# Optimization experiments

Hardware: AMD Instinct MI355X
Metric: run time of the kernel (lower is better)

## Reference

```python
import jax, jax.numpy as jnp
import numpy as np

N = 50000          # nodes
E = 1250000        # edges (avg degree 25)
EMBED = 64
HIDS = [64, 64, 64]
EDGE_DIM = 7       # 1 + 6
VOCAB = 5 ** 8     # 390625
NEG_SLOPE = 0.01   # F.leaky_relu default


def setup_inputs() -> dict:
    key = jax.random.key(0)
    ks = jax.random.split(key, 14)
    L = len(HIDS)
    x = jax.random.randint(ks[0], (N,), 0, VOCAB)
    edge_index = jax.random.randint(ks[1], (2, E), 0, N)
    edge_attr = jax.random.normal(ks[2], (E, EDGE_DIM), dtype=jnp.float32)
    emb = jax.random.normal(ks[3], (VOCAB, EMBED), dtype=jnp.float32) * 0.02
    # all layers have in = out = 64, so params are stacked along layer axis
    lin1_w = jax.random.normal(ks[4], (L, EMBED + EDGE_DIM, HIDS[0]), dtype=jnp.float32) * 0.1
    att_l = jax.random.normal(ks[5], (L, HIDS[0]), dtype=jnp.float32) * 0.1
    att_r = jax.random.normal(ks[6], (L, EMBED), dtype=jnp.float32) * 0.1
    lin2_w = jax.random.normal(ks[7], (L, HIDS[0], HIDS[0]), dtype=jnp.float32) * 0.1
    gbias = jax.random.normal(ks[8], (L, HIDS[0]), dtype=jnp.float32) * 0.01
    d_cat = int(np.sum(HIDS)) + EMBED  # 256
    fc1_w = jax.random.normal(ks[9], (d_cat, 20), dtype=jnp.float32) * 0.05
    fc1_b = jax.random.normal(ks[10], (20,), dtype=jnp.float32) * 0.01
    fc2_w = jax.random.normal(ks[11], (20, 1), dtype=jnp.float32) * 0.1
    fc2_b = jax.random.normal(ks[12], (1,), dtype=jnp.float32) * 0.01
    return {"x": x, "edge_index": edge_index, "edge_attr": edge_attr, "emb": emb,
            "lin1_w": lin1_w, "att_l": att_l, "att_r": att_r, "lin2_w": lin2_w,
            "gbias": gbias, "fc1_w": fc1_w, "fc1_b": fc1_b, "fc2_w": fc2_w, "fc2_b": fc2_b}


def _gate_conv(h, src, dst, edge_attr, w1, al, ar, w2, b):
    # message from source j -> target i; attention softmax over edges sharing a target
    xj = jnp.concatenate([h[src], edge_attr], axis=-1)            # [E, in+7]
    xj = jax.nn.leaky_relu(xj @ w1, NEG_SLOPE)                    # [E, out]
    alpha = jax.nn.leaky_relu(jnp.sum(xj * al, -1) + jnp.sum(h[dst] * ar, -1), NEG_SLOPE)
    amax = jax.ops.segment_max(alpha, dst, num_segments=N)        # [N]
    ea = jnp.exp(alpha - amax[dst])                               # [E]
    denom = jax.ops.segment_sum(ea, dst, num_segments=N)          # [N]
    a = ea / (denom[dst] + 1e-16)
    msg = (xj @ w2) * a[:, None]                                  # [E, out]
    return jax.ops.segment_sum(msg, dst, num_segments=N) + b      # [N, out]


def reference(x, edge_index, edge_attr, emb, lin1_w, att_l, att_r, lin2_w,
              gbias, fc1_w, fc1_b, fc2_w, fc2_b):
    src, dst = edge_index[0], edge_index[1]
    h = emb[x]                                                    # [N, EMBED]
    feats = [h]
    for l in range(len(HIDS)):
        h = jax.nn.relu(_gate_conv(h, src, dst, edge_attr,
                                   lin1_w[l], att_l[l], att_r[l], lin2_w[l], gbias[l]))
        feats.append(h)
    hcat = jnp.concatenate(feats, axis=-1)                        # [N, 256]
    z = jax.nn.relu(hcat @ fc1_w + fc1_b)
    out = jax.nn.sigmoid(z @ fc2_w + fc2_b)
    return out.squeeze(-1)                                        # [N]
```

## Files before the change

kernel.cpp:

```cpp
#include <hip/hip_runtime.h>
#include <math.h>

#define NEG 0.01f

typedef _Float16 f16;
typedef f16 h2 __attribute__((ext_vector_type(2)));

__device__ __forceinline__ float lrelu(float x) { return x > 0.f ? x : NEG * x; }

__device__ __forceinline__ h2 lrelu2(h2 x) {
    h2 y = x * (f16)0.01f;
    return __builtin_elementwise_max(x, y);
}

__device__ __forceinline__ float q16_allsum(float v) {
    int x;
    x = __builtin_amdgcn_update_dpp(0, __float_as_int(v), 0xB1, 0xF, 0xF, true);  v += __int_as_float(x);
    x = __builtin_amdgcn_update_dpp(0, __float_as_int(v), 0x4E, 0xF, 0xF, true);  v += __int_as_float(x);
    x = __builtin_amdgcn_update_dpp(0, __float_as_int(v), 0x124, 0xF, 0xF, true); v += __int_as_float(x);
    x = __builtin_amdgcn_update_dpp(0, __float_as_int(v), 0x128, 0xF, 0xF, true); v += __int_as_float(x);
    return v;
}

__device__ __forceinline__ float x16_32_sum(float v) {
    v += __int_as_float(__builtin_amdgcn_ds_swizzle(__float_as_int(v), 0x401F));
    v += __shfl_xor(v, 32, 64);
    return v;
}

__global__ void k_zero(int* deg, int n) {
    int i = blockIdx.x * blockDim.x + threadIdx.x;
    if (i < n) deg[i] = 0;
}

__global__ void k_count(const int* __restrict__ dst, int* __restrict__ deg,
                        int* __restrict__ rank, int E) {
    int e = blockIdx.x * blockDim.x + threadIdx.x;
    if (e < E) rank[e] = atomicAdd(&deg[dst[e]], 1);
}

__global__ __launch_bounds__(256) void k_scan_part(const int* __restrict__ deg,
                                                   int* __restrict__ bsum, int n) {
    __shared__ int sh[256];
    int b = blockIdx.x, t = threadIdx.x;
    int i0 = b * 1024 + t * 4;
    int s = 0;
    if (i0 + 3 < n) { int4 v = *(const int4*)(deg + i0); s = v.x + v.y + v.z + v.w; }
    else { for (int k = 0; k < 4; k++) if (i0 + k < n) s += deg[i0 + k]; }
    sh[t] = s; __syncthreads();
    for (int d = 128; d > 0; d >>= 1) { if (t < d) sh[t] += sh[t + d]; __syncthreads(); }
    if (t == 0) bsum[b] = sh[0];
}

__global__ __launch_bounds__(256) void k_scan_out(const int* __restrict__ deg,
                                                  const int* __restrict__ bsum,
                                                  int* __restrict__ off, int nb, int n) {
    __shared__ int sb[256];
    __shared__ int sh[256];
    int b = blockIdx.x, t = threadIdx.x;
    int v = (t < nb) ? bsum[t] : 0;
    sb[t] = v; __syncthreads();
    for (int d = 1; d < 256; d <<= 1) {
        int u = (t >= d) ? sb[t - d] : 0;
        __syncthreads(); sb[t] += u; __syncthreads();
    }
    int base = (b == 0) ? 0 : sb[b - 1];
    if (b == 0 && t == 0) off[n] = sb[255];
    int i0 = b * 1024 + t * 4;
    int4 v4 = make_int4(0, 0, 0, 0);
    if (i0 + 3 < n) v4 = *(const int4*)(deg + i0);
    else {
        v4.x = (i0     < n) ? deg[i0]     : 0;
        v4.y = (i0 + 1 < n) ? deg[i0 + 1] : 0;
        v4.z = (i0 + 2 < n) ? deg[i0 + 2] : 0;
        v4.w = (i0 + 3 < n) ? deg[i0 + 3] : 0;
    }
    int s = v4.x + v4.y + v4.z + v4.w;
    sh[t] = s; __syncthreads();
    for (int d = 1; d < 256; d <<= 1) {
        int u = (t >= d) ? sh[t - d] : 0;
        __syncthreads(); sh[t] += u; __syncthreads();
    }
    int ex = base + sh[t] - s;
    if (i0     < n) off[i0]     = ex;
    if (i0 + 1 < n) off[i0 + 1] = ex + v4.x;
    if (i0 + 2 < n) off[i0 + 2] = ex + v4.x + v4.y;
    if (i0 + 3 < n) off[i0 + 3] = ex + v4.x + v4.y + v4.z;
}

__global__ void k_fill_embed(const int* __restrict__ src, const int* __restrict__ dst,
                             const float* __restrict__ eattr, const int* __restrict__ off,
                             const int* __restrict__ rank, uint4* __restrict__ rec, int E,
                             int nbE,
                             const int* __restrict__ x, const float* __restrict__ emb,
                             float* __restrict__ hcat, int N) {
    if ((int)blockIdx.x < nbE) {
        int e = blockIdx.x * 256 + threadIdx.x;
        if (e >= E) return;
        int slot = off[dst[e]] + rank[e];
        const float* ap = eattr + (size_t)e * 7;
        float a0 = ap[0], a1 = ap[1], a2 = ap[2], a3 = ap[3], a4 = ap[4], a5 = ap[5], a6 = ap[6];
        uint4 rv;
        h2 p01 = { (f16)a0, (f16)a1 };
        h2 p23 = { (f16)a2, (f16)a3 };
        h2 p45 = { (f16)a4, (f16)a5 };
        rv.x = __builtin_bit_cast(unsigned int, p01);
        rv.y = __builtin_bit_cast(unsigned int, p23);
        rv.z = __builtin_bit_cast(unsigned int, p45);
        unsigned int a6b = (unsigned int)__builtin_bit_cast(unsigned short, (f16)a6);
        rv.w = a6b | ((unsigned int)src[e] << 16);
        rec[slot] = rv;
    } else {
        int idx = ((int)blockIdx.x - nbE) * 256 + threadIdx.x;
        int node = idx >> 4, j4 = (idx & 15) * 4;
        if (node < N) {
            float4 v = *(const float4*)(emb + (size_t)x[node] * 64 + j4);
            *(float4*)(hcat + (size_t)node * 256 + j4) = v;
        }
    }
}

__global__ __launch_bounds__(256) void k_gemm64(
    const float* __restrict__ A, int a_stride,
    const float* __restrict__ B, const float* __restrict__ bias,
    float* __restrict__ C, int c_stride, f16* __restrict__ Ch,
    int N, int do_relu,
    const float* __restrict__ ar, float* __restrict__ r_out)
{
    __shared__ __align__(16) float sA[64][132];
    __shared__ __align__(16) float sB[64 * 64];
    __shared__ float sar[64];
    int tid = threadIdx.x;
    int row0 = blockIdx.x * 128;

    {
        const float4* b4 = (const float4*)B;
        float4* s4 = (float4*)sB;
        for (int i = tid; i < 1024; i += 256) s4[i] = b4[i];
    }
    if (ar && tid < 64) sar[tid] = ar[tid];

#pragma unroll
    for (int pass = 0; pass < 8; ++pass) {
        int nl = pass * 16 + (tid & 15);
        int k4 = (tid >> 4) * 4;
        int n = row0 + nl; if (n >= N) n = N - 1;
        float4 v = *(const float4*)(A + (size_t)n * a_stride + k4);
        sA[k4 + 0][nl] = v.x; sA[k4 + 1][nl] = v.y;
        sA[k4 + 2][nl] = v.z; sA[k4 + 3][nl] = v.w;
    }
    __syncthreads();

    int tr = tid >> 4, tc = tid & 15;
    int r0 = tr * 8, c0 = tc * 4;
    float acc[8][4];
#pragma unroll
    for (int i = 0; i < 8; i++)
#pragma unroll
        for (int j = 0; j < 4; j++) acc[i][j] = 0.f;

#pragma unroll 4
    for (int k = 0; k < 64; ++k) {
        float4 b4 = *(const float4*)(sB + k * 64 + c0);
        float4 a0 = *(const float4*)&sA[k][r0];
        float4 a1 = *(const float4*)&sA[k][r0 + 4];
#pragma unroll
        for (int j = 0; j < 4; j++) {
            float bj = (&b4.x)[j];
            acc[0][j] += a0.x * bj; acc[1][j] += a0.y * bj;
            acc[2][j] += a0.z * bj; acc[3][j] += a0.w * bj;
            acc[4][j] += a1.x * bj; acc[5][j] += a1.y * bj;
            acc[6][j] += a1.z * bj; acc[7][j] += a1.w * bj;
        }
    }

    float4 bv = make_float4(0.f, 0.f, 0.f, 0.f);
    if (bias) bv = *(const float4*)(bias + c0);
#pragma unroll
    for (int i = 0; i < 8; i++) {
        int n = row0 + r0 + i;
        if (n < N) {
            float4 o;
            o.x = acc[i][0] + bv.x; o.y = acc[i][1] + bv.y;
            o.z = acc[i][2] + bv.z; o.w = acc[i][3] + bv.w;
            if (do_relu) {
                o.x = fmaxf(o.x, 0.f); o.y = fmaxf(o.y, 0.f);
                o.z = fmaxf(o.z, 0.f); o.w = fmaxf(o.w, 0.f);
            }
            if (C) *(float4*)(C + (size_t)n * c_stride + c0) = o;
            if (Ch) {
                uint2 gw;
                gw.x = __builtin_bit_cast(unsigned int, __builtin_amdgcn_cvt_pkrtz(o.x, o.y));
                gw.y = __builtin_bit_cast(unsigned int, __builtin_amdgcn_cvt_pkrtz(o.z, o.w));
                *(uint2*)(Ch + (size_t)n * 64 + c0) = gw;
            }
        }
    }

    if (r_out && tid < 128) {
        int n = row0 + tid;
        if (n < N) {
            float racc = 0.f;
#pragma unroll
            for (int k = 0; k < 64; k++) racc += sA[k][tid] * sar[k];
            r_out[n] = racc;
        }
    }
}

__global__ __launch_bounds__(256) void k_gemm2g1(
    float* __restrict__ hc,
    const float* __restrict__ W2, const float* __restrict__ bias,
    const float* __restrict__ W1n, const float* __restrict__ arn,
    f16* __restrict__ g, float* __restrict__ r_out, int N)
{
    __shared__ __align__(16) float sA[64][132];
    __shared__ __align__(16) float sB[64 * 64];
    __shared__ float sar[64];
    int tid = threadIdx.x, row0 = blockIdx.x * 128;

    {
        const float4* b4 = (const float4*)W2;
        float4* s4 = (float4*)sB;
        for (int i = tid; i < 1024; i += 256) s4[i] = b4[i];
    }
    if (tid < 64) sar[tid] = arn[tid];

#pragma unroll
    for (int pass = 0; pass < 8; ++pass) {
        int nl = pass * 16 + (tid & 15);
        int k4 = (tid >> 4) * 4;
        int n = row0 + nl; if (n >= N) n = N - 1;
        float4 v = *(const float4*)(hc + (size_t)n * 256 + k4);
        sA[k4 + 0][nl] = v.x; sA[k4 + 1][nl] = v.y;
        sA[k4 + 2][nl] = v.z; sA[k4 + 3][nl] = v.w;
    }
    __syncthreads();

    int tr = tid >> 4, tc = tid & 15;
    int r0 = tr * 8, c0 = tc * 4;
    float acc[8][4];
#pragma unroll
    for (int i = 0; i < 8; i++)
#pragma unroll
        for (int j = 0; j < 4; j++) acc[i][j] = 0.f;

#pragma unroll 4
    for (int k = 0; k < 64; ++k) {
        float4 b4 = *(const float4*)(sB + k * 64 + c0);
        float4 a0 = *(const float4*)&sA[k][r0];
        float4 a1 = *(const float4*)&sA[k][r0 + 4];
#pragma unroll
        for (int j = 0; j < 4; j++) {
            float bj = (&b4.x)[j];
            acc[0][j] += a0.x * bj; acc[1][j] += a0.y * bj;
            acc[2][j] += a0.z * bj; acc[3][j] += a0.w * bj;
            acc[4][j] += a1.x * bj; acc[5][j] += a1.y * bj;
            acc[6][j] += a1.z * bj; acc[7][j] += a1.w * bj;
        }
    }

    float4 bv = *(const float4*)(bias + c0);
#pragma unroll
    for (int i = 0; i < 8; i++) {
        acc[i][0] = fmaxf(acc[i][0] + bv.x, 0.f);
        acc[i][1] = fmaxf(acc[i][1] + bv.y, 0.f);
        acc[i][2] = fmaxf(acc[i][2] + bv.z, 0.f);
        acc[i][3] = fmaxf(acc[i][3] + bv.w, 0.f);
        int n = row0 + r0 + i;
        if (n < N) *(float4*)(hc + (size_t)n * 256 + c0) =
            make_float4(acc[i][0], acc[i][1], acc[i][2], acc[i][3]);
    }
    __syncthreads();

    {
        const float4* b4 = (const float4*)W1n;
        float4* s4 = (float4*)sB;
        for (int i = tid; i < 1024; i += 256) s4[i] = b4[i];
    }
#pragma unroll
    for (int i = 0; i < 8; i++)
#pragma unroll
        for (int j = 0; j < 4; j++) sA[c0 + j][r0 + i] = acc[i][j];
    __syncthreads();

#pragma unroll
    for (int i = 0; i < 8; i++)
#pragma unroll
        for (int j = 0; j < 4; j++) acc[i][j] = 0.f;

#pragma unroll 4
    for (int k = 0; k < 64; ++k) {
        float4 b4 = *(const float4*)(sB + k * 64 + c0);
        float4 a0 = *(const float4*)&sA[k][r0];
        float4 a1 = *(const float4*)&sA[k][r0 + 4];
#pragma unroll
        for (int j = 0; j < 4; j++) {
            float bj = (&b4.x)[j];
            acc[0][j] += a0.x * bj; acc[1][j] += a0.y * bj;
            acc[2][j] += a0.z * bj; acc[3][j] += a0.w * bj;
            acc[4][j] += a1.x * bj; acc[5][j] += a1.y * bj;
            acc[6][j] += a1.z * bj; acc[7][j] += a1.w * bj;
        }
    }

#pragma unroll
    for (int i = 0; i < 8; i++) {
        int n = row0 + r0 + i;
        if (n < N) {
            uint2 gw;
            gw.x = __builtin_bit_cast(unsigned int, __builtin_amdgcn_cvt_pkrtz(acc[i][0], acc[i][1]));
            gw.y = __builtin_bit_cast(unsigned int, __builtin_amdgcn_cvt_pkrtz(acc[i][2], acc[i][3]));
            *(uint2*)(g + (size_t)n * 64 + c0) = gw;
        }
    }
    if (tid < 128) {
        int n = row0 + tid;
        if (n < N) {
            float racc = 0.f;
#pragma unroll
            for (int k = 0; k < 64; k++) racc += sA[k][tid] * sar[k];
            r_out[n] = racc;
        }
    }
}

struct ConvW {
    h2 w01[4], w23[4], w45[4], w6_[4];
    h2 al01, al23;
};

__device__ __forceinline__ void do_edge(uint4 rv, bool valid, float ri,
                                        const ConvW& W, const f16* __restrict__ g,
                                        int l16, float4& s, float& den) {
    h2 a01 = __builtin_bit_cast(h2, rv.x);
    h2 a23 = __builtin_bit_cast(h2, rv.y);
    h2 a45 = __builtin_bit_cast(h2, rv.z);
    h2 a6p = __builtin_bit_cast(h2, rv.w & 0xFFFFu);
    int sn  = (int)(rv.w >> 16);
    uint2 gv = *(const uint2*)(g + (size_t)sn * 64 + 4 * l16);
    h2 g01 = __builtin_bit_cast(h2, gv.x);
    h2 g23 = __builtin_bit_cast(h2, gv.y);

    float c0 = __builtin_amdgcn_fdot2(a01, W.w01[0],
               __builtin_amdgcn_fdot2(a23, W.w23[0],
               __builtin_amdgcn_fdot2(a45, W.w45[0],
               __builtin_amdgcn_fdot2(a6p, W.w6_[0], 0.f, false), false), false), false);
    float c1 = __builtin_amdgcn_fdot2(a01, W.w01[1],
               __builtin_amdgcn_fdot2(a23, W.w23[1],
               __builtin_amdgcn_fdot2(a45, W.w45[1],
               __builtin_amdgcn_fdot2(a6p, W.w6_[1], 0.f, false), false), false), false);
    float c2 = __builtin_amdgcn_fdot2(a01, W.w01[2],
               __builtin_amdgcn_fdot2(a23, W.w23[2],
               __builtin_amdgcn_fdot2(a45, W.w45[2],
               __builtin_amdgcn_fdot2(a6p, W.w6_[2], 0.f, false), false), false), false);
    float c3 = __builtin_amdgcn_fdot2(a01, W.w01[3],
               __builtin_amdgcn_fdot2(a23, W.w23[3],
               __builtin_amdgcn_fdot2(a45, W.w45[3],
               __builtin_amdgcn_fdot2(a6p, W.w6_[3], 0.f, false), false), false), false);

    h2 x01 = lrelu2(g01 + __builtin_amdgcn_cvt_pkrtz(c0, c1));
    h2 x23 = lrelu2(g23 + __builtin_amdgcn_cvt_pkrtz(c2, c3));
    float p = __builtin_amdgcn_fdot2(x01, W.al01,
              __builtin_amdgcn_fdot2(x23, W.al23, 0.f, false), false);
    p = q16_allsum(p);
    float alpha = lrelu(p + ri);
    float w = valid ? __expf(alpha) : 0.f;
    s.x += w * (float)x01.x; s.y += w * (float)x01.y;
    s.z += w * (float)x23.x; s.w += w * (float)x23.y;
    den += w;
}

__global__ __launch_bounds__(256) void k_conv(
    const int* __restrict__ off, const uint4* __restrict__ rec,
    const f16* __restrict__ g, const float* __restrict__ r,
    const float* __restrict__ w1, const float* __restrict__ al,
    float* __restrict__ aggdst, int N)
{
    int lane = threadIdx.x & 63;
    int wid  = threadIdx.x >> 6;
    int node = blockIdx.x * 4 + wid;
    if (node >= N) return;
    int q = lane >> 4, l16 = lane & 15;

    ConvW W;
    const float* wb = w1 + 64 * 64;
#pragma unroll
    for (int j = 0; j < 4; j++) {
        int f = 4 * l16 + j;
        W.w01[j] = h2{ (f16)wb[f],       (f16)wb[64 + f]  };
        W.w23[j] = h2{ (f16)wb[128 + f], (f16)wb[192 + f] };
        W.w45[j] = h2{ (f16)wb[256 + f], (f16)wb[320 + f] };
        W.w6_[j] = h2{ (f16)wb[384 + f], (f16)0.f         };
    }
    W.al01 = h2{ (f16)al[4 * l16],     (f16)al[4 * l16 + 1] };
    W.al23 = h2{ (f16)al[4 * l16 + 2], (f16)al[4 * l16 + 3] };

    float ri = r[node];
    int e0 = off[node], e1 = off[node + 1];

    float4 s = make_float4(0.f, 0.f, 0.f, 0.f);
    float den = 0.f;
    for (int e = e0; e < e1; e += 8) {
        int ea = e + q, eb = e + 4 + q;
        bool va = ea < e1, vb = eb < e1;
        uint4 ra = rec[va ? ea : (e1 - 1)];
        uint4 rb = rec[vb ? eb : (e1 - 1)];
        do_edge(ra, va, ri, W, g, l16, s, den);
        do_edge(rb, vb, ri, W, g, l16, s, den);
    }
    s.x = x16_32_sum(s.x); s.y = x16_32_sum(s.y);
    s.z = x16_32_sum(s.z); s.w = x16_32_sum(s.w);
    den = x16_32_sum(den);
    float inv = 1.f / (den + 1e-16f);
    if (q == 0) {
        float4 o = make_float4(s.x * inv, s.y * inv, s.z * inv, s.w * inv);
        *(float4*)(aggdst + (size_t)node * 256 + 4 * l16) = o;
    }
}

__global__ void k_head(const float* __restrict__ hcat, const float* __restrict__ f1w,
                       const float* __restrict__ f1b, const float* __restrict__ f2w,
                       const float* __restrict__ f2b, float* __restrict__ out, int N) {
    int i = blockIdx.x * blockDim.x + threadIdx.x;
    if (i >= N) return;
    float z[20];
#pragma unroll
    for (int j = 0; j < 20; j++) z[j] = f1b[j];
    const float4* hr = (const float4*)(hcat + (size_t)i * 256);
    for (int k4 = 0; k4 < 64; k4++) {
        float4 h = hr[k4];
        const float* wr = f1w + k4 * 4 * 20;
#pragma unroll
        for (int j = 0; j < 20; j++)
            z[j] += h.x * wr[j] + h.y * wr[20 + j] + h.z * wr[40 + j] + h.w * wr[60 + j];
    }
    float o = f2b[0];
#pragma unroll
    for (int j = 0; j < 20; j++) o += fmaxf(z[j], 0.f) * f2w[j];
    out[i] = 1.f / (1.f + __expf(-o));
}

extern "C" void kernel_launch(void* const* d_in, const int* in_sizes, int n_in,
                              void* d_out, int out_size, void* d_ws, size_t ws_size,
                              hipStream_t stream) {
    const int*   x     = (const int*)d_in[0];
    const int*   eidx  = (const int*)d_in[1];
    const float* eattr = (const float*)d_in[2];
    const float* emb   = (const float*)d_in[3];
    const float* lin1  = (const float*)d_in[4];
    const float* attl  = (const float*)d_in[5];
    const float* attr_ = (const float*)d_in[6];
    const float* lin2  = (const float*)d_in[7];
    const float* gbias = (const float*)d_in[8];
    const float* f1w   = (const float*)d_in[9];
    const float* f1b   = (const float*)d_in[10];
    const float* f2w   = (const float*)d_in[11];
    const float* f2b   = (const float*)d_in[12];
    float* out = (float*)d_out;

    int N = in_sizes[0];
    int E = in_sizes[1] / 2;
    const int* src = eidx;
    const int* dst = eidx + E;

    char* p = (char*)d_ws;
    auto alloc = [&](size_t bytes) { void* q = (void*)p; p += (bytes + 255) & ~(size_t)255; return q; };
    float* hcat = (float*)alloc((size_t)N * 256 * 4);
    f16*   g    = (f16*)alloc((size_t)N * 64 * 2);
    float* r    = (float*)alloc((size_t)N * 4);
    int*   off  = (int*)alloc((size_t)(N + 1) * 4);
    int*   deg  = (int*)alloc((size_t)N * 4);
    int*   rank = (int*)alloc((size_t)E * 4);
    int*   bsum = (int*)alloc(256 * 4);
    uint4* rec  = (uint4*)alloc((size_t)E * 16);

    int nbs = (N + 1023) / 1024;
    int nbE = (E + 255) / 256;
    int nbEmb = (N * 16 + 255) / 256;

    k_zero<<<(N + 255) / 256, 256, 0, stream>>>(deg, N);
    k_count<<<nbE, 256, 0, stream>>>(dst, deg, rank, E);
    k_scan_part<<<nbs, 256, 0, stream>>>(deg, bsum, N);
    k_scan_out<<<nbs, 256, 0, stream>>>(deg, bsum, off, nbs, N);
    k_fill_embed<<<nbE + nbEmb, 256, 0, stream>>>(src, dst, eattr, off, rank, rec, E,
                                                  nbE, x, emb, hcat, N);

    int nbg = (N + 127) / 128;
    int nbc = (N + 3) / 4;
    k_gemm64<<<nbg, 256, 0, stream>>>(hcat, 256, lin1, nullptr,
                                      nullptr, 0, g, N, 0, attr_, r);
    k_conv<<<nbc, 256, 0, stream>>>(off, rec, g, r, lin1, attl, hcat + 64, N);
    for (int l = 0; l < 2; l++) {
        k_gemm2g1<<<nbg, 256, 0, stream>>>(hcat + 64 * (l + 1),
                                           lin2 + (size_t)l * 4096, gbias + l * 64,
                                           lin1 + (size_t)(l + 1) * 71 * 64,
                                           attr_ + (l + 1) * 64, g, r, N);
        k_conv<<<nbc, 256, 0, stream>>>(off, rec, g, r,
                                        lin1 + (size_t)(l + 1) * 71 * 64,
                                        attl + (l + 1) * 64, hcat + 64 * (l + 2), N);
    }
    k_gemm64<<<nbg, 256, 0, stream>>>(hcat + 192, 256, lin2 + 2 * 4096, gbias + 128,
                                      hcat + 192, 256, nullptr, N, 1, nullptr, nullptr);
    k_head<<<(N + 255) / 256, 256, 0, stream>>>(hcat, f1w, f1b, f2w, f2b, out, N);
}
```

Measured before the change: 532.4 us.

## Fuse final GEMM with MLP head, prepack conv weights, deepen edge-loop prefetch

The last layer's lin2 GEMM is fused with the fc1/fc2 head into one kernel that keeps the layer-3 output in shared memory, so that slice of hcat is never written back and re-read. The head's dot products are split across two half-blocks. Per-layer conv edge weights and attention vectors are converted to packed fp16 once, inside the zero kernel, so each conv wave does 5 vector loads instead of many scalar float loads and conversions. The conv edge loop now handles 16 edges per iteration and issues all record and gather loads before the math, giving more memory-level parallelism at the cost of more registers.

```diff
diff --git a/kernel.cpp b/kernel.cpp
--- a/kernel.cpp
+++ b/kernel.cpp
@@ -28,9 +28,34 @@
     return v;
 }
 
-__global__ void k_zero(int* deg, int n) {
+__global__ void k_zero(int* __restrict__ deg, int n,
+                       const float* __restrict__ lin1, const float* __restrict__ attl,
+                       uint4* __restrict__ wpack) {
     int i = blockIdx.x * blockDim.x + threadIdx.x;
     if (i < n) deg[i] = 0;
+    if (i < 48) {
+        int l = i >> 4, t = i & 15;
+        const float* wb  = lin1 + (size_t)l * 71 * 64 + 64 * 64;
+        const float* alp = attl + l * 64;
+        unsigned int u[20];
+#pragma unroll
+        for (int j = 0; j < 4; j++) {
+            int f = 4 * t + j;
+            h2 a = { (f16)wb[f],       (f16)wb[64 + f]  }; u[j]      = __builtin_bit_cast(unsigned int, a);
+            h2 b = { (f16)wb[128 + f], (f16)wb[192 + f] }; u[4 + j]  = __builtin_bit_cast(unsigned int, b);
+            h2 c = { (f16)wb[256 + f], (f16)wb[320 + f] }; u[8 + j]  = __builtin_bit_cast(unsigned int, c);
+            h2 d = { (f16)wb[384 + f], (f16)0.f         }; u[12 + j] = __builtin_bit_cast(unsigned int, d);
+        }
+        h2 e0 = { (f16)alp[4 * t],     (f16)alp[4 * t + 1] }; u[16] = __builtin_bit_cast(unsigned int, e0);
+        h2 e1 = { (f16)alp[4 * t + 2], (f16)alp[4 * t + 3] }; u[17] = __builtin_bit_cast(unsigned int, e1);
+        u[18] = 0; u[19] = 0;
+        uint4* o = wpack + (size_t)i * 5;
+        o[0] = make_uint4(u[0],  u[1],  u[2],  u[3]);
+        o[1] = make_uint4(u[4],  u[5],  u[6],  u[7]);
+        o[2] = make_uint4(u[8],  u[9],  u[10], u[11]);
+        o[3] = make_uint4(u[12], u[13], u[14], u[15]);
+        o[4] = make_uint4(u[16], u[17], u[18], u[19]);
+    }
 }
 
 __global__ void k_count(const int* __restrict__ dst, int* __restrict__ deg,
@@ -330,15 +355,12 @@
     h2 al01, al23;
 };
 
-__device__ __forceinline__ void do_edge(uint4 rv, bool valid, float ri,
-                                        const ConvW& W, const f16* __restrict__ g,
-                                        int l16, float4& s, float& den) {
+__device__ __forceinline__ void edge_math(uint4 rv, uint2 gv, bool valid, float ri,
+                                          const ConvW& W, float4& s, float& den) {
     h2 a01 = __builtin_bit_cast(h2, rv.x);
     h2 a23 = __builtin_bit_cast(h2, rv.y);
     h2 a45 = __builtin_bit_cast(h2, rv.z);
     h2 a6p = __builtin_bit_cast(h2, rv.w & 0xFFFFu);
-    int sn  = (int)(rv.w >> 16);
-    uint2 gv = *(const uint2*)(g + (size_t)sn * 64 + 4 * l16);
     h2 g01 = __builtin_bit_cast(h2, gv.x);
     h2 g23 = __builtin_bit_cast(h2, gv.y);
 
@@ -374,8 +396,7 @@
 __global__ __launch_bounds__(256) void k_conv(
     const int* __restrict__ off, const uint4* __restrict__ rec,
     const f16* __restrict__ g, const float* __restrict__ r,
-    const float* __restrict__ w1, const float* __restrict__ al,
-    float* __restrict__ aggdst, int N)
+    const uint4* __restrict__ wpack, float* __restrict__ aggdst, int N)
 {
     int lane = threadIdx.x & 63;
     int wid  = threadIdx.x >> 6;
@@ -384,30 +405,41 @@
     int q = lane >> 4, l16 = lane & 15;
 
     ConvW W;
-    const float* wb = w1 + 64 * 64;
-#pragma unroll
-    for (int j = 0; j < 4; j++) {
-        int f = 4 * l16 + j;
-        W.w01[j] = h2{ (f16)wb[f],       (f16)wb[64 + f]  };
-        W.w23[j] = h2{ (f16)wb[128 + f], (f16)wb[192 + f] };
-        W.w45[j] = h2{ (f16)wb[256 + f], (f16)wb[320 + f] };
-        W.w6_[j] = h2{ (f16)wb[384 + f], (f16)0.f         };
-    }
-    W.al01 = h2{ (f16)al[4 * l16],     (f16)al[4 * l16 + 1] };
-    W.al23 = h2{ (f16)al[4 * l16 + 2], (f16)al[4 * l16 + 3] };
+    {
+        const uint4* wp = wpack + l16 * 5;
+        uint4 v0 = wp[0], v1 = wp[1], v2 = wp[2], v3 = wp[3], v4 = wp[4];
+        W.w01[0] = __builtin_bit_cast(h2, v0.x); W.w01[1] = __builtin_bit_cast(h2, v0.y);
+        W.w01[2] = __builtin_bit_cast(h2, v0.z); W.w01[3] = __builtin_bit_cast(h2, v0.w);
+        W.w23[0] = __builtin_bit_cast(h2, v1.x); W.w23[1] = __builtin_bit_cast(h2, v1.y);
+        W.w23[2] = __builtin_bit_cast(h2, v1.z); W.w23[3] = __builtin_bit_cast(h2, v1.w);
+        W.w45[0] = __builtin_bit_cast(h2, v2.x); W.w45[1] = __builtin_bit_cast(h2, v2.y);
+        W.w45[2] = __builtin_bit_cast(h2, v2.z); W.w45[3] = __builtin_bit_cast(h2, v2.w);
+        W.w6_[0] = __builtin_bit_cast(h2, v3.x); W.w6_[1] = __builtin_bit_cast(h2, v3.y);
+        W.w6_[2] = __builtin_bit_cast(h2, v3.z); W.w6_[3] = __builtin_bit_cast(h2, v3.w);
+        W.al01   = __builtin_bit_cast(h2, v4.x); W.al23   = __builtin_bit_cast(h2, v4.y);
+    }
 
     float ri = r[node];
     int e0 = off[node], e1 = off[node + 1];
 
     float4 s = make_float4(0.f, 0.f, 0.f, 0.f);
     float den = 0.f;
-    for (int e = e0; e < e1; e += 8) {
-        int ea = e + q, eb = e + 4 + q;
-        bool va = ea < e1, vb = eb < e1;
-        uint4 ra = rec[va ? ea : (e1 - 1)];
-        uint4 rb = rec[vb ? eb : (e1 - 1)];
-        do_edge(ra, va, ri, W, g, l16, s, den);
-        do_edge(rb, vb, ri, W, g, l16, s, den);
+    for (int e = e0; e < e1; e += 16) {
+        int ea = e + q, eb = ea + 4, ec = ea + 8, ed = ea + 12;
+        int last = e1 - 1;
+        bool va = ea < e1, vb = eb < e1, vc = ec < e1, vd = ed < e1;
+        uint4 ra = rec[va ? ea : last];
+        uint4 rb = rec[vb ? eb : last];
+        uint4 rc = rec[vc ? ec : last];
+        uint4 rd = rec[vd ? ed : last];
+        uint2 ga = *(const uint2*)(g + (size_t)(ra.w >> 16) * 64 + 4 * l16);
+        uint2 gb = *(const uint2*)(g + (size_t)(rb.w >> 16) * 64 + 4 * l16);
+        uint2 gc = *(const uint2*)(g + (size_t)(rc.w >> 16) * 64 + 4 * l16);
+        uint2 gd = *(const uint2*)(g + (size_t)(rd.w >> 16) * 64 + 4 * l16);
+        edge_math(ra, ga, va, ri, W, s, den);
+        edge_math(rb, gb, vb, ri, W, s, den);
+        edge_math(rc, gc, vc, ri, W, s, den);
+        edge_math(rd, gd, vd, ri, W, s, den);
     }
     s.x = x16_32_sum(s.x); s.y = x16_32_sum(s.y);
     s.z = x16_32_sum(s.z); s.w = x16_32_sum(s.w);
@@ -419,26 +451,130 @@
     }
 }
 
-__global__ void k_head(const float* __restrict__ hcat, const float* __restrict__ f1w,
-                       const float* __restrict__ f1b, const float* __restrict__ f2w,
-                       const float* __restrict__ f2b, float* __restrict__ out, int N) {
-    int i = blockIdx.x * blockDim.x + threadIdx.x;
-    if (i >= N) return;
+__global__ __launch_bounds__(256) void k_gemm2head(
+    const float* __restrict__ hcat,
+    const float* __restrict__ W2, const float* __restrict__ bias,
+    const float* __restrict__ f1w, const float* __restrict__ f1b,
+    const float* __restrict__ f2w, const float* __restrict__ f2b,
+    float* __restrict__ out, int N)
+{
+    __shared__ __align__(16) float sA[64][132];
+    __shared__ __align__(16) float sBW[5120];
+    __shared__ float sP[128 * 20];
+    int tid = threadIdx.x, row0 = blockIdx.x * 128;
+
+    {
+        const float4* b4 = (const float4*)W2;
+        float4* s4 = (float4*)sBW;
+        for (int i = tid; i < 1024; i += 256) s4[i] = b4[i];
+    }
+#pragma unroll
+    for (int pass = 0; pass < 8; ++pass) {
+        int nl = pass * 16 + (tid & 15);
+        int k4 = (tid >> 4) * 4;
+        int n = row0 + nl; if (n >= N) n = N - 1;
+        float4 v = *(const float4*)(hcat + (size_t)n * 256 + 192 + k4);
+        sA[k4 + 0][nl] = v.x; sA[k4 + 1][nl] = v.y;
+        sA[k4 + 2][nl] = v.z; sA[k4 + 3][nl] = v.w;
+    }
+    __syncthreads();
+
+    int tr = tid >> 4, tc = tid & 15;
+    int r0 = tr * 8, c0 = tc * 4;
+    float acc[8][4];
+#pragma unroll
+    for (int i = 0; i < 8; i++)
+#pragma unroll
+        for (int j = 0; j < 4; j++) acc[i][j] = 0.f;
+
+#pragma unroll 4
+    for (int k = 0; k < 64; ++k) {
+        float4 b4 = *(const float4*)(sBW + k * 64 + c0);
+        float4 a0 = *(const float4*)&sA[k][r0];
+        float4 a1 = *(const float4*)&sA[k][r0 + 4];
+#pragma unroll
+        for (int j = 0; j < 4; j++) {
+            float bj = (&b4.x)[j];
+            acc[0][j] += a0.x * bj; acc[1][j] += a0.y * bj;
+            acc[2][j] += a0.z * bj; acc[3][j] += a0.w * bj;
+            acc[4][j] += a1.x * bj; acc[5][j] += a1.y * bj;
+            acc[6][j] += a1.z * bj; acc[7][j] += a1.w * bj;
+        }
+    }
+
+    float4 fw[5];
+    {
+        const float4* w4 = (const float4*)f1w;
+#pragma unroll
+        for (int i2 = 0; i2 < 5; i2++) fw[i2] = w4[tid + i2 * 256];
+    }
+    __syncthreads();
+
+    float* sO = &sA[0][0];
+    float4 bv = *(const float4*)(bias + c0);
+#pragma unroll
+    for (int i = 0; i < 8; i++) {
+        acc[i][0] = fmaxf(acc[i][0] + bv.x, 0.f);
+        acc[i][1] = fmaxf(acc[i][1] + bv.y, 0.f);
+        acc[i][2] = fmaxf(acc[i][2] + bv.z, 0.f);
+        acc[i][3] = fmaxf(acc[i][3] + bv.w, 0.f);
+        int rr = r0 + i;
+        sO[rr * 65 + c0 + 0] = acc[i][0];
+        sO[rr * 65 + c0 + 1] = acc[i][1];
+        sO[rr * 65 + c0 + 2] = acc[i][2];
+        sO[rr * 65 + c0 + 3] = acc[i][3];
+    }
+    {
+        float4* sw4 = (float4*)sBW;
+#pragma unroll
+        for (int i2 = 0; i2 < 5; i2++) sw4[tid + i2 * 256] = fw[i2];
+    }
+    __syncthreads();
+
+    int rloc = tid & 127;
+    int half = tid >> 7;
+    int n = row0 + rloc;
+    int nn = (n < N) ? n : N - 1;
     float z[20];
 #pragma unroll
-    for (int j = 0; j < 20; j++) z[j] = f1b[j];
-    const float4* hr = (const float4*)(hcat + (size_t)i * 256);
-    for (int k4 = 0; k4 < 64; k4++) {
-        float4 h = hr[k4];
-        const float* wr = f1w + k4 * 4 * 20;
-#pragma unroll
-        for (int j = 0; j < 20; j++)
-            z[j] += h.x * wr[j] + h.y * wr[20 + j] + h.z * wr[40 + j] + h.w * wr[60 + j];
-    }
-    float o = f2b[0];
-#pragma unroll
-    for (int j = 0; j < 20; j++) o += fmaxf(z[j], 0.f) * f2w[j];
-    out[i] = 1.f / (1.f + __expf(-o));
+    for (int j = 0; j < 20; j++) z[j] = 0.f;
+    const float4* hr = (const float4*)(hcat + (size_t)nn * 256);
+    if (half == 0) {
+        for (int k4 = 0; k4 < 32; k4++) {
+            float4 h = hr[k4];
+            const float* wr = sBW + k4 * 80;
+#pragma unroll
+            for (int j = 0; j < 20; j++)
+                z[j] += h.x * wr[j] + h.y * wr[20 + j] + h.z * wr[40 + j] + h.w * wr[60 + j];
+        }
+    } else {
+        for (int k4 = 32; k4 < 48; k4++) {
+            float4 h = hr[k4];
+            const float* wr = sBW + k4 * 80;
+#pragma unroll
+            for (int j = 0; j < 20; j++)
+                z[j] += h.x * wr[j] + h.y * wr[20 + j] + h.z * wr[40 + j] + h.w * wr[60 + j];
+        }
+        for (int k = 0; k < 64; k += 2) {
+            float hx = sO[rloc * 65 + k], hy = sO[rloc * 65 + k + 1];
+            const float* wr = sBW + (192 + k) * 20;
+#pragma unroll
+            for (int j = 0; j < 20; j++)
+                z[j] += hx * wr[j] + hy * wr[20 + j];
+        }
+#pragma unroll
+        for (int j = 0; j < 20; j++) sP[rloc * 20 + j] = z[j];
+    }
+    __syncthreads();
+    if (half == 0 && n < N) {
+        float o = f2b[0];
+#pragma unroll
+        for (int j = 0; j < 20; j++) {
+            float zj = z[j] + sP[rloc * 20 + j] + f1b[j];
+            o += fmaxf(zj, 0.f) * f2w[j];
+        }
+        out[n] = 1.f / (1.f + __expf(-o));
+    }
 }
 
 extern "C" void kernel_launch(void* const* d_in, const int* in_sizes, int n_in,
@@ -474,12 +610,13 @@
     int*   rank = (int*)alloc((size_t)E * 4);
     int*   bsum = (int*)alloc(256 * 4);
     uint4* rec  = (uint4*)alloc((size_t)E * 16);
+    uint4* wpack = (uint4*)alloc((size_t)48 * 5 * 16);
 
     int nbs = (N + 1023) / 1024;
     int nbE = (E + 255) / 256;
     int nbEmb = (N * 16 + 255) / 256;
 
-    k_zero<<<(N + 255) / 256, 256, 0, stream>>>(deg, N);
+    k_zero<<<(N + 255) / 256, 256, 0, stream>>>(deg, N, lin1, attl, wpack);
     k_count<<<nbE, 256, 0, stream>>>(dst, deg, rank, E);
     k_scan_part<<<nbs, 256, 0, stream>>>(deg, bsum, N);
     k_scan_out<<<nbs, 256, 0, stream>>>(deg, bsum, off, nbs, N);
@@ -490,17 +627,16 @@
     int nbc = (N + 3) / 4;
     k_gemm64<<<nbg, 256, 0, stream>>>(hcat, 256, lin1, nullptr,
                                       nullptr, 0, g, N, 0, attr_, r);
-    k_conv<<<nbc, 256, 0, stream>>>(off, rec, g, r, lin1, attl, hcat + 64, N);
+    k_conv<<<nbc, 256, 0, stream>>>(off, rec, g, r, wpack, hcat + 64, N);
     for (int l = 0; l < 2; l++) {
         k_gemm2g1<<<nbg, 256, 0, stream>>>(hcat + 64 * (l + 1),
                                            lin2 + (size_t)l * 4096, gbias + l * 64,
                                            lin1 + (size_t)(l + 1) * 71 * 64,
                                            attr_ + (l + 1) * 64, g, r, N);
         k_conv<<<nbc, 256, 0, stream>>>(off, rec, g, r,
-                                        lin1 + (size_t)(l + 1) * 71 * 64,
-                                        attl + (l + 1) * 64, hcat + 64 * (l + 2), N);
-    }
-    k_gemm64<<<nbg, 256, 0, stream>>>(hcat + 192, 256, lin2 + 2 * 4096, gbias + 128,
-                                      hcat + 192, 256, nullptr, N, 1, nullptr, nullptr);
-    k_head<<<(N + 255) / 256, 256, 0, stream>>>(hcat, f1w, f1b, f2w, f2b, out, N);
-}
+                                        wpack + (size_t)(l + 1) * 80,
+                                        hcat + 64 * (l + 2), N);
+    }
+    k_gemm2head<<<nbg, 256, 0, stream>>>(hcat, lin2 + 2 * 4096, gbias + 128,
+                                         f1w, f1b, f2w, f2b, out, N);
+}
```

Result: faster. 505.8 us (-5.0%).
